# Performance work log

Hardware: AMD Instinct MI355X
Metric: run time of the kernel (lower is better)

The kernel has to match this reference:

```python
import jax, jax.numpy as jnp
import numpy as np

U1 = 512
U2 = 512
BATCH = 8192
INPUT_DIM = (U1 + U2) * 3  # 3072
UNITS = U2 * 3             # 1536


def _build_mask():
    """Replicates the block-structured random 0/1 unit_diags construction.

    Unit blocks (rows): [0,U2), [U2,2U2), [2U2,3U2).
    Input blocks (cols): ds1,ds2,ds3 of width U1 each, then stn1,stn2,stn3 of width U2.
    Each (unit-block, input-block) pair has a fixed Bernoulli keep-probability
    derived from the original randint(2)/randint(4) logic.
    """
    rng = np.random.default_rng(0)
    col_edges = [0, U1, 2 * U1, 3 * U1, 3 * U1 + U2, 3 * U1 + 2 * U2, 3 * U1 + 3 * U2]
    # keep-probabilities per unit-block (rows) x input-block (cols)
    probs = [
        [1.0, 0.5, 0.0, 1.0, 0.5, 0.0],   # units [0, U2)
        [0.5, 0.75, 0.5, 0.5, 0.75, 0.5], # units [U2, 2U2): randint(4)>0 -> p=0.75
        [0.0, 0.5, 1.0, 0.0, 0.5, 1.0],   # units [2U2, 3U2)
    ]
    p = np.zeros((UNITS, INPUT_DIM), dtype=np.float32)
    for ub in range(3):
        for j in range(6):
            p[ub * U2:(ub + 1) * U2, col_edges[j]:col_edges[j + 1]] = probs[ub][j]
    mask = (rng.random((UNITS, INPUT_DIM)) < p).astype(np.float32)
    return mask


def setup_inputs() -> dict:
    key = jax.random.key(0)
    k1, k2 = jax.random.split(key)
    x = jax.random.normal(k1, (BATCH, INPUT_DIM), dtype=jnp.float32)
    # w_init = uniform(0, 0.01), non-negative constrained
    w = jax.random.uniform(k2, (INPUT_DIM, UNITS), dtype=jnp.float32, minval=0.0, maxval=0.01)
    # gpi_bias = [0, 0] -> bias initialized to zeros
    b = jnp.zeros((UNITS,), dtype=jnp.float32)
    mask = jnp.asarray(_build_mask())  # (UNITS, INPUT_DIM), fixed 0/1 constants
    return {"x": x, "w": w, "b": b, "mask": mask}


def reference(x, w, b, mask):
    # Original: p[b,u,:] = mask[u,:] * x[b,:] ;  f = diag_part(p @ w) + b
    # => f[b,u] = sum_i mask[u,i] * x[b,i] * w[i,u] + b[u]
    # Collapses to a masked linear: x @ (mask.T * w) + b
    return x @ (mask.T * w) + b
```

## Files before the change

kernel.cpp:

```cpp
#include <hip/hip_runtime.h>
#include <stdint.h>

#define MDIM 8192
#define NDIM 1536
#define KDIM 3072

#define BM 128
#define BN 128
#define BK 32

typedef unsigned short u16;
typedef float  f32x4  __attribute__((ext_vector_type(4)));
typedef __bf16 bf16x8 __attribute__((ext_vector_type(8)));

__device__ __forceinline__ u16 f2bf(float f) {
    union { float f; unsigned int u; } v; v.f = f;
    unsigned int u = v.u;
    return (u16)((u + 0x7fffu + ((u >> 16) & 1u)) >> 16);
}

__global__ void cvt_x_kernel(const float4* __restrict__ x, ushort4* __restrict__ xb) {
    int i = blockIdx.x * 256 + threadIdx.x;
    float4 v = x[i];
    ushort4 o;
    o.x = f2bf(v.x); o.y = f2bf(v.y); o.z = f2bf(v.z); o.w = f2bf(v.w);
    xb[i] = o;
}

__global__ void make_b_kernel(const float* __restrict__ w, const float* __restrict__ mask,
                              u16* __restrict__ Bt) {
    __shared__ float sw[64][65];
    const int t  = threadIdx.x;
    const int kb = blockIdx.x % (KDIM / 64);
    const int nb = blockIdx.x / (KDIM / 64);
    const int k0 = kb * 64, n0 = nb * 64;

    {
        const int c4 = t & 15;
        const int r  = t >> 4;
#pragma unroll
        for (int rr = 0; rr < 4; ++rr) {
            int row = rr * 16 + r;
            float4 v = *(const float4*)&w[(size_t)(k0 + row) * NDIM + n0 + c4 * 4];
            sw[row][c4 * 4 + 0] = v.x;
            sw[row][c4 * 4 + 1] = v.y;
            sw[row][c4 * 4 + 2] = v.z;
            sw[row][c4 * 4 + 3] = v.w;
        }
    }
    __syncthreads();
    {
        const int n  = t >> 2;
        const int ks = (t & 3) * 16;
#pragma unroll
        for (int j = 0; j < 4; ++j) {
            int k = ks + j * 4;
            float4 mv = *(const float4*)&mask[(size_t)(n0 + n) * KDIM + k0 + k];
            ushort4 o;
            o.x = f2bf(mv.x * sw[k + 0][n]);
            o.y = f2bf(mv.y * sw[k + 1][n]);
            o.z = f2bf(mv.z * sw[k + 2][n]);
            o.w = f2bf(mv.w * sw[k + 3][n]);
            *(ushort4*)&Bt[(size_t)(n0 + n) * KDIM + k0 + k] = o;
        }
    }
}

__device__ __forceinline__ void gload_lds16(const u16* g, u16* l) {
    __builtin_amdgcn_global_load_lds(
        (const __attribute__((address_space(1))) unsigned int*)g,
        (__attribute__((address_space(3))) unsigned int*)l, 16, 0, 0);
}

__global__ void gemm_kernel(const u16* __restrict__ A,
                            const u16* __restrict__ B,
                            const float* __restrict__ bias,
                            float* __restrict__ C) {
    __shared__ u16 sA[BM * BK];
    __shared__ u16 sB[BN * BK];

    const int tid  = threadIdx.x;
    const int wave = tid >> 6;
    const int lane = tid & 63;

    const int bx = blockIdx.x % (NDIM / BN);
    const int by = blockIdx.x / (NDIM / BN);
    const int m0 = by * BM, n0 = bx * BN;

    const int srow = lane >> 2;
    const int scol = (lane & 3) * 8;

    const int wm = (wave >> 1) * 64;
    const int wn = (wave & 1) * 64;
    const int fr = lane & 15;
    const int fq = lane >> 4;

    f32x4 acc[4][4] = {};

    const u16* gA0 = A + (size_t)(m0 + wave * 16 + srow) * KDIM + scol;
    const u16* gB0 = B + (size_t)(n0 + wave * 16 + srow) * KDIM + scol;
    u16* lA0 = &sA[(wave * 16) * BK];
    u16* lA1 = &sA[(wave * 16 + 64) * BK];
    u16* lB0 = &sB[(wave * 16) * BK];
    u16* lB1 = &sB[(wave * 16 + 64) * BK];

    for (int k0 = 0; k0 < KDIM; k0 += BK) {
        __syncthreads();
        gload_lds16(gA0 + k0,                      lA0);
        gload_lds16(gA0 + k0 + (size_t)64 * KDIM,  lA1);
        gload_lds16(gB0 + k0,                      lB0);
        gload_lds16(gB0 + k0 + (size_t)64 * KDIM,  lB1);
        __syncthreads();

        bf16x8 af[4], bfv[4];
#pragma unroll
        for (int mt = 0; mt < 4; ++mt)
            af[mt] = *(const bf16x8*)&sA[(wm + mt * 16 + fr) * BK + fq * 8];
#pragma unroll
        for (int nt = 0; nt < 4; ++nt)
            bfv[nt] = *(const bf16x8*)&sB[(wn + nt * 16 + fr) * BK + fq * 8];
#pragma unroll
        for (int mt = 0; mt < 4; ++mt)
#pragma unroll
            for (int nt = 0; nt < 4; ++nt)
                acc[mt][nt] = __builtin_amdgcn_mfma_f32_16x16x32_bf16(
                    af[mt], bfv[nt], acc[mt][nt], 0, 0, 0);
    }

#pragma unroll
    for (int nt = 0; nt < 4; ++nt) {
        int n = n0 + wn + nt * 16 + fr;
        float bv = bias[n];
#pragma unroll
        for (int mt = 0; mt < 4; ++mt) {
            int m = m0 + wm + mt * 16 + fq * 4;
#pragma unroll
            for (int r = 0; r < 4; ++r)
                C[(size_t)(m + r) * NDIM + n] = acc[mt][nt][r] + bv;
        }
    }
}

extern "C" void kernel_launch(void* const* d_in, const int* in_sizes, int n_in,
                              void* d_out, int out_size, void* d_ws, size_t ws_size,
                              hipStream_t stream) {
    const float* x    = (const float*)d_in[0];
    const float* w    = (const float*)d_in[1];
    const float* bias = (const float*)d_in[2];
    const float* mask = (const float*)d_in[3];
    float* out = (float*)d_out;

    u16* xb = (u16*)d_ws;
    u16* Bt = (u16*)((char*)d_ws + (size_t)50331648);

    cvt_x_kernel<<<(MDIM * KDIM / 4) / 256, 256, 0, stream>>>(
        (const float4*)x, (ushort4*)xb);
    make_b_kernel<<<(KDIM / 64) * (NDIM / 64), 256, 0, stream>>>(w, mask, Bt);
    gemm_kernel<<<(MDIM / BM) * (NDIM / BN), 256, 0, stream>>>(xb, Bt, bias, out);
}
```

Measured before the change: 287.1 us.

## Fuse fp32-to-bf16 conversion of x into GEMM and add XOR LDS swizzle

Drops the separate cvt_x pass. The GEMM now loads fp32 x tiles straight into LDS through global_load_lds and converts them to bf16 in registers before the MFMA. This removes a full read and write of the 100MB activation plus one kernel launch. In exchange, the GEMM reads twice the A bytes from global memory on every tile reload, and it adds XOR swizzles on the A and B LDS layouts to avoid bank conflicts.

```diff
diff --git a/kernel.cpp b/kernel.cpp
--- a/kernel.cpp
+++ b/kernel.cpp
@@ -19,14 +19,6 @@
     return (u16)((u + 0x7fffu + ((u >> 16) & 1u)) >> 16);
 }
 
-__global__ void cvt_x_kernel(const float4* __restrict__ x, ushort4* __restrict__ xb) {
-    int i = blockIdx.x * 256 + threadIdx.x;
-    float4 v = x[i];
-    ushort4 o;
-    o.x = f2bf(v.x); o.y = f2bf(v.y); o.z = f2bf(v.z); o.w = f2bf(v.w);
-    xb[i] = o;
-}
-
 __global__ void make_b_kernel(const float* __restrict__ w, const float* __restrict__ mask,
                               u16* __restrict__ Bt) {
     __shared__ float sw[64][65];
@@ -34,7 +26,6 @@
     const int kb = blockIdx.x % (KDIM / 64);
     const int nb = blockIdx.x / (KDIM / 64);
     const int k0 = kb * 64, n0 = nb * 64;
-
     {
         const int c4 = t & 15;
         const int r  = t >> 4;
@@ -66,18 +57,18 @@
     }
 }
 
-__device__ __forceinline__ void gload_lds16(const u16* g, u16* l) {
+__device__ __forceinline__ void gload_lds16(const void* g, void* l) {
     __builtin_amdgcn_global_load_lds(
         (const __attribute__((address_space(1))) unsigned int*)g,
         (__attribute__((address_space(3))) unsigned int*)l, 16, 0, 0);
 }
 
-__global__ void gemm_kernel(const u16* __restrict__ A,
+__global__ void gemm_kernel(const float* __restrict__ X,
                             const u16* __restrict__ B,
                             const float* __restrict__ bias,
                             float* __restrict__ C) {
-    __shared__ u16 sA[BM * BK];
-    __shared__ u16 sB[BN * BK];
+    __shared__ float sA[BM * BK];
+    __shared__ u16   sB[BN * BK];
 
     const int tid  = threadIdx.x;
     const int wave = tid >> 6;
@@ -87,38 +78,55 @@
     const int by = blockIdx.x / (NDIM / BN);
     const int m0 = by * BM, n0 = bx * BN;
 
-    const int srow = lane >> 2;
-    const int scol = (lane & 3) * 8;
+    const int arow  = lane >> 3;
+    const int acol  = ((lane & 7) ^ (lane >> 3)) * 4;
+
+    const int bsrow = lane >> 2;
+    const int bscol = ((lane & 3) ^ ((lane >> 3) & 3)) * 8;
 
     const int wm = (wave >> 1) * 64;
     const int wn = (wave & 1) * 64;
     const int fr = lane & 15;
     const int fq = lane >> 4;
+    const int fswB = (fq ^ ((fr >> 1) & 3)) * 8;
+    const int s0   = ((2 * fq) ^ (fr & 7)) * 4;
+    const int s1   = (((2 * fq) | 1) ^ (fr & 7)) * 4;
 
     f32x4 acc[4][4] = {};
 
-    const u16* gA0 = A + (size_t)(m0 + wave * 16 + srow) * KDIM + scol;
-    const u16* gB0 = B + (size_t)(n0 + wave * 16 + srow) * KDIM + scol;
-    u16* lA0 = &sA[(wave * 16) * BK];
-    u16* lA1 = &sA[(wave * 16 + 64) * BK];
+    const float* gA0 = X + (size_t)(m0 + wave * 32 + arow) * KDIM + acol;
+    const u16*   gB0 = B + (size_t)(n0 + wave * 16 + bsrow) * KDIM + bscol;
+    float* lA0 = &sA[(wave * 32 +  0) * BK];
+    float* lA1 = &sA[(wave * 32 +  8) * BK];
+    float* lA2 = &sA[(wave * 32 + 16) * BK];
+    float* lA3 = &sA[(wave * 32 + 24) * BK];
     u16* lB0 = &sB[(wave * 16) * BK];
     u16* lB1 = &sB[(wave * 16 + 64) * BK];
 
     for (int k0 = 0; k0 < KDIM; k0 += BK) {
         __syncthreads();
         gload_lds16(gA0 + k0,                      lA0);
-        gload_lds16(gA0 + k0 + (size_t)64 * KDIM,  lA1);
+        gload_lds16(gA0 + k0 + (size_t) 8 * KDIM,  lA1);
+        gload_lds16(gA0 + k0 + (size_t)16 * KDIM,  lA2);
+        gload_lds16(gA0 + k0 + (size_t)24 * KDIM,  lA3);
         gload_lds16(gB0 + k0,                      lB0);
         gload_lds16(gB0 + k0 + (size_t)64 * KDIM,  lB1);
         __syncthreads();
 
         bf16x8 af[4], bfv[4];
 #pragma unroll
-        for (int mt = 0; mt < 4; ++mt)
-            af[mt] = *(const bf16x8*)&sA[(wm + mt * 16 + fr) * BK + fq * 8];
+        for (int mt = 0; mt < 4; ++mt) {
+            const int r = wm + mt * 16 + fr;
+            f32x4 lo = *(const f32x4*)&sA[r * BK + s0];
+            f32x4 hi = *(const f32x4*)&sA[r * BK + s1];
+            bf16x8 a;
+#pragma unroll
+            for (int e = 0; e < 4; ++e) { a[e] = (__bf16)lo[e]; a[4 + e] = (__bf16)hi[e]; }
+            af[mt] = a;
+        }
 #pragma unroll
         for (int nt = 0; nt < 4; ++nt)
-            bfv[nt] = *(const bf16x8*)&sB[(wn + nt * 16 + fr) * BK + fq * 8];
+            bfv[nt] = *(const bf16x8*)&sB[(wn + nt * 16 + fr) * BK + fswB];
 #pragma unroll
         for (int mt = 0; mt < 4; ++mt)
 #pragma unroll
@@ -150,11 +158,8 @@
     const float* mask = (const float*)d_in[3];
     float* out = (float*)d_out;
 
-    u16* xb = (u16*)d_ws;
-    u16* Bt = (u16*)((char*)d_ws + (size_t)50331648);
+    u16* Bt = (u16*)d_ws;
 
-    cvt_x_kernel<<<(MDIM * KDIM / 4) / 256, 256, 0, stream>>>(
-        (const float4*)x, (ushort4*)xb);
     make_b_kernel<<<(KDIM / 64) * (NDIM / 64), 256, 0, stream>>>(w, mask, Bt);
-    gemm_kernel<<<(MDIM / BM) * (NDIM / BN), 256, 0, stream>>>(xb, Bt, bias, out);
+    gemm_kernel<<<(MDIM / BM) * (NDIM / BN), 256, 0, stream>>>(x, Bt, bias, out);
 }
```

New measurement: 319.9 us. 11.4% more time.
